# Optimization experiments

Hardware: AMD Instinct MI355X
Metric: run time of the kernel (lower is better)

## Reference

```python
import jax, jax.numpy as jnp
import numpy as np

HEADS = 3
FILT = 16
V_FEATS = 11
N_NODES = 100000
E_INT = 400000
E_NH = 1600000
ATT_SIZE = FILT * 2 * HEADS            # 96
DENSE_IN = ATT_SIZE * HEADS            # 288


def setup_inputs() -> dict:
    key = jax.random.key(0)
    ks = jax.random.split(key, 12)
    node_feats = jax.random.normal(ks[0], (N_NODES, V_FEATS), dtype=jnp.float32)
    edge_int = jax.random.randint(ks[1], (2, E_INT), 0, N_NODES, dtype=jnp.int64)
    edge_nh = jax.random.randint(ks[2], (2, E_NH), 0, N_NODES, dtype=jnp.int64)
    s = 0.1
    W_int = jax.random.normal(ks[3], (V_FEATS, HEADS * FILT), dtype=jnp.float32) * s
    a_src_int = jax.random.normal(ks[4], (HEADS, FILT), dtype=jnp.float32) * s
    a_dst_int = jax.random.normal(ks[5], (HEADS, FILT), dtype=jnp.float32) * s
    W_nh = jax.random.normal(ks[6], (V_FEATS, HEADS * FILT), dtype=jnp.float32) * s
    a_src_nh = jax.random.normal(ks[7], (HEADS, FILT), dtype=jnp.float32) * s
    a_dst_nh = jax.random.normal(ks[8], (HEADS, FILT), dtype=jnp.float32) * s
    att_w = jax.random.normal(ks[9], (ATT_SIZE, HEADS), dtype=jnp.float32) * s
    dense_w = jax.random.normal(ks[10], (DENSE_IN, 1), dtype=jnp.float32) * s
    dense_b = jnp.zeros((1,), dtype=jnp.float32)
    return {
        "node_feats": node_feats,
        "W_int": W_int, "a_src_int": a_src_int, "a_dst_int": a_dst_int,
        "W_nh": W_nh, "a_src_nh": a_src_nh, "a_dst_nh": a_dst_nh,
        "att_w": att_w, "dense_w": dense_w, "dense_b": dense_b,
        "edge_int": edge_int, "edge_nh": edge_nh,
    }


def _gat(x, edges, W, a_src, a_dst):
    """Graph-attention branch: gather -> edge softmax (per dst) -> scatter-add."""
    n = x.shape[0]
    h = (x @ W).reshape(n, HEADS, FILT)              # [N,H,F]
    src, dst = edges[0], edges[1]
    e_s = jnp.einsum('nhf,hf->nh', h, a_src)         # [N,H]
    e_d = jnp.einsum('nhf,hf->nh', h, a_dst)
    e = jax.nn.leaky_relu(e_s[src] + e_d[dst], 0.2)  # [E,H]
    m = jax.ops.segment_max(e, dst, num_segments=n)  # per-dst max for stability
    m = jnp.where(jnp.isfinite(m), m, 0.0)
    p = jnp.exp(e - m[dst])
    denom = jax.ops.segment_sum(p, dst, num_segments=n)
    alpha = p / (denom[dst] + 1e-16)                 # [E,H]
    out = jax.ops.segment_sum(alpha[:, :, None] * h[src], dst, num_segments=n)
    return out.reshape(n, HEADS * FILT)              # [N,48]


def reference(node_feats, W_int, a_src_int, a_dst_int, W_nh, a_src_nh, a_dst_nh,
              att_w, dense_w, dense_b, edge_int, edge_nh):
    x_int = _gat(node_feats, edge_int, W_int, a_src_int, a_dst_int)   # [N,48]
    x_nh = _gat(node_feats, edge_nh, W_nh, a_src_nh, a_dst_nh)        # [N,48]
    x = jnp.concatenate((x_int, x_nh), axis=1)                        # [N,96]
    # multi-head self-attention pooling over nodes
    scores = jnp.tanh(x @ att_w)                                      # [N,3]
    alpha = jax.nn.softmax(scores, axis=0)                            # softmax over nodes
    rep = jnp.einsum('nh,nd->hd', alpha, x).reshape(-1)               # [288]
    out = rep @ dense_w + dense_b                                     # [1]
    return out
```

## Files before the change

### kernel.cpp

```cpp
#include <hip/hip_runtime.h>
#include <math.h>

#define HEADS 3
#define FILT 16
#define HF 48
#define VF 11

#define NBGP 2048
#define NBINMAX 512
#define CAP0 4096
#define CAP1 8192
#define SCCH 8192

typedef unsigned int uint;
typedef unsigned short ushort;

__device__ inline uint f2bf(float x) {
    uint u = __float_as_uint(x);
    return (u + 0x7FFFu + ((u >> 16) & 1u)) >> 16;
}

__device__ inline float tanh_fast(float s) {
    const float sc = fminf(fmaxf(s, -15.f), 15.f);
    const float t = __expf(2.f * sc);
    return (t - 1.f) / (t + 1.f);
}


__global__ __launch_bounds__(256) void k_nodes(
    const float* __restrict__ nf,
    const float* __restrict__ W_int, const float* __restrict__ as_int, const float* __restrict__ ad_int,
    const float* __restrict__ W_nh,  const float* __restrict__ as_nh,  const float* __restrict__ ad_nh,
    float* __restrict__ ws, int* __restrict__ binfill, int N)
{
    __shared__ float sW0[VF*HF], sW1[VF*HF];
    __shared__ float sa[4][HF];
    __shared__ float sF[64*VF];
    __shared__ uint  sH[64*32];
    const int t = threadIdx.x;
    for (int i = t; i < VF*HF; i += 256) { sW0[i] = W_int[i]; sW1[i] = W_nh[i]; }
    if (t < HF) { sa[0][t] = as_int[t]; sa[1][t] = ad_int[t]; sa[2][t] = as_nh[t]; sa[3][t] = ad_nh[t]; }

    const long Nl = N;
    const long B0 = (long)blockIdx.x * 64;
    {
        const long idx = (long)blockIdx.x * 256 + t;
        if (idx < 2*NBINMAX) binfill[idx] = 0;
    }
    for (int i = t; i < 64*VF; i += 256) {
        const long g = B0*VF + i;
        sF[i] = (g < Nl*VF) ? nf[g] : 0.f;
    }
    __syncthreads();

    const int nl = t >> 2;
    const int q  = t & 3;
    const long n = B0 + nl;
    const bool valid = n < Nl;

    float f[VF];
    #pragma unroll
    for (int v = 0; v < VF; v++) f[v] = sF[nl*VF + v];

    for (int b = 0; b < 2; b++) {
        if (b == 1) __syncthreads();
        const float* W = b ? sW1 : sW0;
        float acc[12];
        #pragma unroll
        for (int j = 0; j < 12; j++) acc[j] = 0.f;
        #pragma unroll
        for (int v = 0; v < VF; v++) {
            const float fv = f[v];
            #pragma unroll
            for (int j = 0; j < 12; j++)
                acc[j] = fmaf(fv, W[v*HF + q*12 + j], acc[j]);
        }
        #pragma unroll
        for (int i = 0; i < 6; i++)
            sH[nl*32 + q*6 + i] = f2bf(acc[2*i]) | (f2bf(acc[2*i+1]) << 16);
        sH[nl*32 + 24 + 2*q + 0] = 0u;
        sH[nl*32 + 24 + 2*q + 1] = 0u;

        float s0=0.f,s1=0.f,s2=0.f,d0=0.f,d1=0.f,d2=0.f;
        #pragma unroll
        for (int j = 0; j < 12; j++) {
            const int fg = q*12 + j;
            const int hd = fg >> 4;
            const float ps = acc[j] * sa[2*b + 0][fg];
            const float pd = acc[j] * sa[2*b + 1][fg];
            s0 += (hd == 0) ? ps : 0.f;  d0 += (hd == 0) ? pd : 0.f;
            s1 += (hd == 1) ? ps : 0.f;  d1 += (hd == 1) ? pd : 0.f;
            s2 += (hd == 2) ? ps : 0.f;  d2 += (hd == 2) ? pd : 0.f;
        }
        s0 += __shfl_xor(s0,1); s0 += __shfl_xor(s0,2);
        s1 += __shfl_xor(s1,1); s1 += __shfl_xor(s1,2);
        s2 += __shfl_xor(s2,1); s2 += __shfl_xor(s2,2);
        d0 += __shfl_xor(d0,1); d0 += __shfl_xor(d0,2);
        d1 += __shfl_xor(d1,1); d1 += __shfl_xor(d1,2);
        d2 += __shfl_xor(d2,1); d2 += __shfl_xor(d2,2);
        if (valid && q == 0) {
            float* ES = ws + 64*Nl + (b ? 8*Nl : 0);
            float* ED = ES + 4*Nl;
            ((float4*)ES)[n] = make_float4(s0, s1, s2, 0.f);
            ((float4*)ED)[n] = make_float4(d0, d1, d2, 0.f);
        }
        __syncthreads();
        uint* Hg = (uint*)(ws + (b ? 32*Nl : 0));
        for (int i = t; i < 64*32; i += 256) {
            const long node = B0 + (i >> 5);
            if (node < Nl) Hg[B0*32 + i] = sH[i];
        }
    }
}

__global__ __launch_bounds__(256) void k_binscatter(
    const int* __restrict__ e0, int E0, int nb0,
    const int* __restrict__ e1, int E1,
    int* __restrict__ binfill, uint* __restrict__ pk0, uint* __restrict__ pk1)
{
    __shared__ int lh[NBINMAX], lb[NBINMAX];
    const int b = blockIdx.x;
    const int* e; long E; int* bf; uint* pk; int bb, cap;
    if (b < nb0) { e = e0; E = E0; bf = binfill;           pk = pk0; bb = b;       cap = CAP0; }
    else         { e = e1; E = E1; bf = binfill + NBINMAX; pk = pk1; bb = b - nb0; cap = CAP1; }
    for (int i = threadIdx.x; i < NBINMAX; i += 256) lh[i] = 0;
    __syncthreads();
    const int t = threadIdx.x;
    const long base = (long)bb * SCCH;
    #pragma unroll 4
    for (int k = 0; k < SCCH/256; k++) {
        const long i = base + (long)k*256 + t;
        if (i < E) atomicAdd(&lh[e[E + i] >> 8], 1);
    }
    __syncthreads();
    for (int i = t; i < NBINMAX; i += 256) {
        const int c = lh[i];
        lb[i] = c ? atomicAdd(&bf[i], c) : 0;
        lh[i] = 0;
    }
    __syncthreads();
    #pragma unroll 4
    for (int k = 0; k < SCCH/256; k++) {
        const long i = base + (long)k*256 + t;
        if (i < E) {
            const int s = e[i];
            const int d = e[E + i];
            const int bin = d >> 8;
            const int off = atomicAdd(&lh[bin], 1);
            pk[(long)bin*cap + lb[bin] + off] = ((uint)(d & 255) << 17) | (uint)s;
        }
    }
}

__global__ __launch_bounds__(256) void k_binbucket(
    const uint* __restrict__ pk0, const uint* __restrict__ pk1,
    const int* __restrict__ binfill, int nbin,
    int2* __restrict__ ms0, int* __restrict__ bk0,
    int2* __restrict__ ms1, int* __restrict__ bk1, int N)
{
    __shared__ int nc[256], ns[256], wsum[4];
    const int b = blockIdx.x;
    const int br = (b < nbin) ? 0 : 1;
    const int bin = b - br*nbin;
    const uint* pk = br ? pk1 : pk0;
    const int cap  = br ? CAP1 : CAP0;
    int2* ms = br ? ms1 : ms0;
    int* bk  = br ? bk1 : bk0;
    const long pbase = (long)bin * cap;
    const int m = binfill[br*NBINMAX + bin];
    const int t = threadIdx.x, lane = t & 63, wid = t >> 6;

    nc[t] = 0;
    __syncthreads();
    for (int i = t; i < m; i += 256)
        atomicAdd(&nc[(pk[pbase + i] >> 17) & 255], 1);
    __syncthreads();
    const int v = nc[t];
    int x = v;
    #pragma unroll
    for (int d = 1; d < 64; d <<= 1) { const int u = __shfl_up(x, d); if (lane >= d) x += u; }
    if (lane == 63) wsum[wid] = x;
    __syncthreads();
    int wb = 0;
    #pragma unroll
    for (int w = 0; w < 4; w++) if (w < wid) wb += wsum[w];
    ns[t] = wb + x - v;
    const int n = bin*256 + t;
    if (n < N) ms[n] = make_int2(v, (int)pbase + ns[t] + v);
    nc[t] = 0;
    __syncthreads();
    for (int i = t; i < m; i += 256) {
        const uint p = pk[pbase + i];
        const int dl = (p >> 17) & 255;
        const int off = atomicAdd(&nc[dl], 1);
        bk[pbase + ns[dl] + off] = (int)(p & 0x1FFFFu);
    }
}

__global__ __launch_bounds__(256) void k_gp(
    const uint* __restrict__ H0, const uint* __restrict__ H1,
    const float* __restrict__ ES0, const float4* __restrict__ ED0,
    const float* __restrict__ ES1, const float4* __restrict__ ED1,
    const int2* __restrict__ ms0, const int* __restrict__ bk0,
    const int2* __restrict__ ms1, const int* __restrict__ bk1,
    const float* __restrict__ att_w, const float* __restrict__ dense_w,
    float* __restrict__ gpart, int N)
{
    __shared__ int   sIdx[4][4*64];
    __shared__ float sP[4][4*192];
    const int t = threadIdx.x, lane = t & 63, wid = t >> 6;
    const int half = lane >> 5;
    const int hl = lane & 31;
    const int hcc = (hl >> 3) < 3 ? (hl >> 3) : 2;

    float cL0[3]={0,0,0}, cH0[3]={0,0,0}, cL1[3]={0,0,0}, cH1[3]={0,0,0};
    if (hl < 24) {
        const int f0 = 2*hl, f1 = f0 + 1;
        #pragma unroll
        for (int k = 0; k < 3; k++) {
            if (half == 0) {
                cL0[k] = att_w[f0*3 + k];        cH0[k] = att_w[f1*3 + k];
                cL1[k] = att_w[(HF+f0)*3 + k];   cH1[k] = att_w[(HF+f1)*3 + k];
            } else {
                cL0[k] = dense_w[k*96 + f0];     cH0[k] = dense_w[k*96 + f1];
                cL1[k] = dense_w[k*96 + HF+f0];  cH1[k] = dense_w[k*96 + HF+f1];
            }
        }
    }

    int* iw = sIdx[wid];
    float* pw = sP[wid];

    float acc6[6] = {0,0,0,0,0,0};
    const int gw = blockIdx.x*4 + wid;
    const int nw = NBGP*4;

    for (int n = gw; n < N; n += 2*nw) {
        const int nB = n + nw;
        const bool hasB = nB < N;
        const int2 m0t = ms0[n];
        const int2 m1t = ms1[n];
        const int2 m2t = hasB ? ms0[nB] : make_int2(0, 0);
        const int2 m3t = hasB ? ms1[nB] : make_int2(0, 0);
        int deg[4] = {m0t.x, m1t.x, m2t.x, m3t.x};
        int bas[4] = {m0t.y - m0t.x, m1t.y - m1t.x, m2t.y - m2t.x, m3t.y - m3t.x};
        const int mx = max(max(deg[0], deg[1]), max(deg[2], deg[3]));

        float xL[4], xH[4];

        if (mx <= 64) {
            float4 ev[4];
            ev[0] = ED0[n]; ev[1] = ED1[n];
            ev[2] = hasB ? ED0[nB] : make_float4(0,0,0,0);
            ev[3] = hasB ? ED1[nB] : make_float4(0,0,0,0);
            int sv[4];
            sv[0] = (lane < deg[0]) ? bk0[bas[0] + lane] : 0;
            sv[1] = (lane < deg[1]) ? bk1[bas[1] + lane] : 0;
            sv[2] = (lane < deg[2]) ? bk0[bas[2] + lane] : 0;
            sv[3] = (lane < deg[3]) ? bk1[bas[3] + lane] : 0;
            float4 es[4];
            es[0] = ((const float4*)ES0)[sv[0]];
            es[1] = ((const float4*)ES1)[sv[1]];
            es[2] = ((const float4*)ES0)[sv[2]];
            es[3] = ((const float4*)ES1)[sv[3]];
            #pragma unroll
            for (int T = 0; T < 4; T++) {
                float v0 = es[T].x + ev[T].x, v1 = es[T].y + ev[T].y, v2 = es[T].z + ev[T].z;
                v0 = fmaxf(v0, 0.2f*v0);
                v1 = fmaxf(v1, 0.2f*v1);
                v2 = fmaxf(v2, 0.2f*v2);
                const bool a = lane < deg[T];
                const float p0 = a ? __expf(v0) : 0.f;
                const float p1 = a ? __expf(v1) : 0.f;
                const float p2 = a ? __expf(v2) : 0.f;
                iw[T*64 + lane] = sv[T];
                pw[T*192 + lane*3 + 0] = p0;
                pw[T*192 + lane*3 + 1] = p1;
                pw[T*192 + lane*3 + 2] = p2;
            }
            float accL[4] = {0,0,0,0}, accH[4] = {0,0,0,0}, den[4] = {0,0,0,0};
            const int R = (mx + 7) >> 3;
            for (int r = 0; r < R; r++) {
                const int j0 = r*8;
                uint w[4][4]; float q[4][4];
                #pragma unroll
                for (int T = 0; T < 4; T++) {
                    const uint* H = (T & 1) ? H1 : H0;
                    if (j0 < deg[T]) {
                        #pragma unroll
                        for (int u = 0; u < 4; u++) {
                            const int ei = j0 + 2*u + half;
                            q[T][u] = pw[T*192 + ei*3 + hcc];
                            w[T][u] = H[(long)iw[T*64 + ei]*32 + hl];
                        }
                    }
                }
                #pragma unroll
                for (int T = 0; T < 4; T++) {
                    if (j0 < deg[T]) {
                        #pragma unroll
                        for (int u = 0; u < 4; u++) {
                            accL[T] = fmaf(q[T][u], __uint_as_float(w[T][u] << 16), accL[T]);
                            accH[T] = fmaf(q[T][u], __uint_as_float(w[T][u] & 0xFFFF0000u), accH[T]);
                            den[T] += q[T][u];
                        }
                    }
                }
            }
            #pragma unroll
            for (int T = 0; T < 4; T++) {
                accL[T] += __shfl_xor(accL[T], 32);
                accH[T] += __shfl_xor(accH[T], 32);
                den[T]  += __shfl_xor(den[T], 32);
                const float dinv = 1.f / (den[T] + 1e-16f);
                xL[T] = accL[T] * dinv;
                xH[T] = accH[T] * dinv;
            }
        } else {
            #pragma unroll
            for (int T = 0; T < 4; T++) {
                const uint* H   = (T & 1) ? H1 : H0;
                const float* ES = (T & 1) ? ES1 : ES0;
                const float4* ED = (T & 1) ? ED1 : ED0;
                const int* bk   = (T & 1) ? bk1 : bk0;
                const int nn    = (T >> 1) ? nB : n;
                float accL = 0.f, accH = 0.f, dn = 0.f;
                if (deg[T] > 0) {
                    const float4 edv = ED[nn];
                    for (int e0 = 0; e0 < deg[T]; e0 += 64) {
                        int m = deg[T] - e0; if (m > 64) m = 64;
                        int srcv = 0; float p0 = 0.f, p1 = 0.f, p2 = 0.f;
                        if (lane < m) {
                            srcv = bk[bas[T] + e0 + lane];
                            const float4 esv = ((const float4*)ES)[srcv];
                            float v0 = esv.x + edv.x, v1 = esv.y + edv.y, v2 = esv.z + edv.z;
                            v0 = fmaxf(v0, 0.2f*v0);
                            v1 = fmaxf(v1, 0.2f*v1);
                            v2 = fmaxf(v2, 0.2f*v2);
                            p0 = __expf(v0); p1 = __expf(v1); p2 = __expf(v2);
                        }
                        iw[lane] = srcv;
                        pw[lane*3 + 0] = p0; pw[lane*3 + 1] = p1; pw[lane*3 + 2] = p2;
                        for (int j = 0; j < m; j += 2) {
                            const int ei = j + half;
                            const float qq = pw[ei*3 + hcc];
                            const uint wv = H[(long)iw[ei]*32 + hl];
                            accL = fmaf(qq, __uint_as_float(wv << 16), accL);
                            accH = fmaf(qq, __uint_as_float(wv & 0xFFFF0000u), accH);
                            dn += qq;
                        }
                    }
                }
                accL += __shfl_xor(accL, 32);
                accH += __shfl_xor(accH, 32);
                dn   += __shfl_xor(dn, 32);
                const float dinv = 1.f / (dn + 1e-16f);
                xL[T] = accL * dinv;
                xH[T] = accH * dinv;
            }
        }

        #pragma unroll
        for (int s = 0; s < 2; s++) {
            if (s == 1 && !hasB) break;
            float rr[3];
            #pragma unroll
            for (int k = 0; k < 3; k++)
                rr[k] = xL[2*s]*cL0[k] + xH[2*s]*cH0[k] + xL[2*s+1]*cL1[k] + xH[2*s+1]*cH1[k];
            #pragma unroll
            for (int k = 0; k < 3; k++) {
                #pragma unroll
                for (int o = 1; o < 32; o <<= 1) rr[k] += __shfl_xor(rr[k], o);
            }
            float oo[3];
            #pragma unroll
            for (int k = 0; k < 3; k++) oo[k] = __shfl_xor(rr[k], 32);
            if (lane == 0) {
                #pragma unroll
                for (int k = 0; k < 3; k++) {
                    const float e = __expf(tanh_fast(rr[k]));
                    acc6[k]   += e;
                    acc6[3+k] += e * oo[k];
                }
            }
        }
    }

    __shared__ float red[4][6];
    if (lane == 0) {
        #pragma unroll
        for (int k = 0; k < 6; k++) red[wid][k] = acc6[k];
    }
    __syncthreads();
    if (t < 6) gpart[(long)blockIdx.x*6 + t] = red[0][t] + red[1][t] + red[2][t] + red[3][t];
}

__global__ __launch_bounds__(1024) void k_final(const float* __restrict__ gpart, int nb,
                                                const float* __restrict__ dense_b,
                                                float* __restrict__ out)
{
    const int t = threadIdx.x, lane = t & 63, wid = t >> 6;
    float acc[6] = {0.f,0.f,0.f,0.f,0.f,0.f};
    for (long i = t; i < nb; i += 1024) {
        #pragma unroll
        for (int k = 0; k < 6; k++) acc[k] += gpart[i*6 + k];
    }
    __shared__ float red[16][6];
    #pragma unroll
    for (int k = 0; k < 6; k++) {
        float v = acc[k];
        #pragma unroll
        for (int o = 32; o > 0; o >>= 1) v += __shfl_xor(v, o);
        if (lane == 0) red[wid][k] = v;
    }
    __syncthreads();
    if (t == 0) {
        float tot[6] = {0.f,0.f,0.f,0.f,0.f,0.f};
        #pragma unroll
        for (int w = 0; w < 16; w++)
            #pragma unroll
            for (int k = 0; k < 6; k++) tot[k] += red[w][k];
        float o = dense_b[0];
        #pragma unroll
        for (int h = 0; h < HEADS; h++) o += tot[3 + h] / tot[h];
        out[0] = o;
    }
}

extern "C" void kernel_launch(void* const* d_in, const int* in_sizes, int n_in,
                              void* d_out, int out_size, void* d_ws, size_t ws_size,
                              hipStream_t stream)
{
    const float* nf      = (const float*)d_in[0];
    const float* W_int   = (const float*)d_in[1];
    const float* as_int  = (const float*)d_in[2];
    const float* ad_int  = (const float*)d_in[3];
    const float* W_nh    = (const float*)d_in[4];
    const float* as_nh   = (const float*)d_in[5];
    const float* ad_nh   = (const float*)d_in[6];
    const float* att_w   = (const float*)d_in[7];
    const float* dense_w = (const float*)d_in[8];
    const float* dense_b = (const float*)d_in[9];
    const int*   e_int   = (const int*)d_in[10];
    const int*   e_nh    = (const int*)d_in[11];

    const int N  = in_sizes[0] / VF;
    const int E0 = in_sizes[10] / 2;
    const int E1 = in_sizes[11] / 2;
    const int nbin = (N + 255) >> 8;

    float* ws = (float*)d_ws;
    const long Nl = N;

    uint* h0 = (uint*)ws;
    uint* h1 = (uint*)(ws + 32*Nl);
    float* es0 = ws + 64*Nl;
    float4* ed0 = (float4*)(ws + 68*Nl);
    float* es1 = ws + 72*Nl;
    float4* ed1 = (float4*)(ws + 76*Nl);
    int2* ms0 = (int2*)(ws + 80*Nl);
    int2* ms1 = (int2*)(ws + 82*Nl);
    int* binfill = (int*)(ws + 84*Nl);
    uint* pk0 = (uint*)(binfill + 2*NBINMAX);
    uint* pk1 = pk0 + (long)nbin*CAP0;
    int* bk0  = (int*)(pk1 + (long)nbin*CAP1);
    int* bk1  = bk0 + (long)nbin*CAP0;
    float* gpart = (float*)(bk1 + (long)nbin*CAP1);

    const int nbK1 = (N + 63) / 64;
    const int nbs0 = (E0 + SCCH - 1) / SCCH;
    const int nbs1 = (E1 + SCCH - 1) / SCCH;

    k_nodes<<<nbK1, 256, 0, stream>>>(nf, W_int, as_int, ad_int, W_nh, as_nh, ad_nh,
                                      ws, binfill, N);
    k_binscatter<<<nbs0 + nbs1, 256, 0, stream>>>(e_int, E0, nbs0, e_nh, E1,
                                                  binfill, pk0, pk1);
    k_binbucket<<<2*nbin, 256, 0, stream>>>(pk0, pk1, binfill, nbin,
                                            ms0, bk0, ms1, bk1, N);
    k_gp<<<NBGP, 256, 0, stream>>>(h0, h1, es0, ed0, es1, ed1,
                                   ms0, bk0, ms1, bk1,
                                   att_w, dense_w, gpart, N);
    k_final<<<1, 1024, 0, stream>>>(gpart, NBGP, dense_b, (float*)d_out);
}
```

Measured before the change: 146.4 us.

## Privatize per-wave bucket counters, halve scatter chunk, prescale gather indices

Bin bucketing now keeps a separate counter histogram for each wave and turns it into per-wave offsets, so LDS atomic contention in the count and scatter passes is spread across four copies and the separate offset array is dropped. The scatter chunk size is halved, which launches more blocks that each do less work. Gather indices are stored pre-shifted by 5 so the inner loop skips a multiply. The costs are extra LDS use, a small extra prefix step, and a different edge order within each bucket, which can change floating-point summation order.

```diff
diff --git a/kernel.cpp b/kernel.cpp
--- a/kernel.cpp
+++ b/kernel.cpp
@@ -10,7 +10,7 @@
 #define NBINMAX 512
 #define CAP0 4096
 #define CAP1 8192
-#define SCCH 8192
+#define SCCH 4096
 
 typedef unsigned int uint;
 typedef unsigned short ushort;
@@ -158,7 +158,7 @@
     int2* __restrict__ ms0, int* __restrict__ bk0,
     int2* __restrict__ ms1, int* __restrict__ bk1, int N)
 {
-    __shared__ int nc[256], ns[256], wsum[4];
+    __shared__ int nc[4][256], wsum[4];
     const int b = blockIdx.x;
     const int br = (b < nbin) ? 0 : 1;
     const int bin = b - br*nbin;
@@ -170,12 +170,13 @@
     const int m = binfill[br*NBINMAX + bin];
     const int t = threadIdx.x, lane = t & 63, wid = t >> 6;
 
-    nc[t] = 0;
+    #pragma unroll
+    for (int r = 0; r < 4; r++) nc[r][t] = 0;
     __syncthreads();
     for (int i = t; i < m; i += 256)
-        atomicAdd(&nc[(pk[pbase + i] >> 17) & 255], 1);
-    __syncthreads();
-    const int v = nc[t];
+        atomicAdd(&nc[wid][(pk[pbase + i] >> 17) & 255], 1);
+    __syncthreads();
+    const int v = nc[0][t] + nc[1][t] + nc[2][t] + nc[3][t];
     int x = v;
     #pragma unroll
     for (int d = 1; d < 64; d <<= 1) { const int u = __shfl_up(x, d); if (lane >= d) x += u; }
@@ -184,16 +185,20 @@
     int wb = 0;
     #pragma unroll
     for (int w = 0; w < 4; w++) if (w < wid) wb += wsum[w];
-    ns[t] = wb + x - v;
+    const int myexcl = wb + x - v;
     const int n = bin*256 + t;
-    if (n < N) ms[n] = make_int2(v, (int)pbase + ns[t] + v);
-    nc[t] = 0;
+    if (n < N) ms[n] = make_int2(v, (int)pbase + myexcl + v);
+    {
+        int s = myexcl;
+        #pragma unroll
+        for (int r = 0; r < 4; r++) { const int c = nc[r][t]; nc[r][t] = s; s += c; }
+    }
     __syncthreads();
     for (int i = t; i < m; i += 256) {
         const uint p = pk[pbase + i];
         const int dl = (p >> 17) & 255;
-        const int off = atomicAdd(&nc[dl], 1);
-        bk[pbase + ns[dl] + off] = (int)(p & 0x1FFFFu);
+        const int off = atomicAdd(&nc[wid][dl], 1);
+        bk[pbase + off] = (int)(p & 0x1FFFFu);
     }
 }
 
@@ -273,7 +278,7 @@
                 const float p0 = a ? __expf(v0) : 0.f;
                 const float p1 = a ? __expf(v1) : 0.f;
                 const float p2 = a ? __expf(v2) : 0.f;
-                iw[T*64 + lane] = sv[T];
+                iw[T*64 + lane] = sv[T] << 5;
                 pw[T*192 + lane*3 + 0] = p0;
                 pw[T*192 + lane*3 + 1] = p1;
                 pw[T*192 + lane*3 + 2] = p2;
@@ -291,7 +296,7 @@
                         for (int u = 0; u < 4; u++) {
                             const int ei = j0 + 2*u + half;
                             q[T][u] = pw[T*192 + ei*3 + hcc];
-                            w[T][u] = H[(long)iw[T*64 + ei]*32 + hl];
+                            w[T][u] = H[(long)iw[T*64 + ei] + hl];
                         }
                     }
                 }
@@ -339,12 +344,12 @@
                             v2 = fmaxf(v2, 0.2f*v2);
                             p0 = __expf(v0); p1 = __expf(v1); p2 = __expf(v2);
                         }
-                        iw[lane] = srcv;
+                        iw[lane] = srcv << 5;
                         pw[lane*3 + 0] = p0; pw[lane*3 + 1] = p1; pw[lane*3 + 2] = p2;
                         for (int j = 0; j < m; j += 2) {
                             const int ei = j + half;
                             const float qq = pw[ei*3 + hcc];
-                            const uint wv = H[(long)iw[ei]*32 + hl];
+                            const uint wv = H[(long)iw[ei] + hl];
                             accL = fmaf(qq, __uint_as_float(wv << 16), accL);
                             accH = fmaf(qq, __uint_as_float(wv & 0xFFFF0000u), accH);
                             dn += qq;
```

Measured after the change: 144.9 us. No clear change (-1.0%).
